# Performance work log

Measured on AMD Instinct MI355X. Metric: run time of the kernel, lower is better.

The kernel has to match this reference:

```python
import jax, jax.numpy as jnp
import numpy as np

B, N, C = 16, 577, 768
H = 12
HD = C // H            # 64 head dim
F = HD // 2            # 32 rotary frequency pairs
END = 24               # sqrt(N - 1): patch grid side
SCALE = HD ** -0.5


def setup_inputs() -> dict:
    key = jax.random.key(0)
    k0, k1, k2, k3 = jax.random.split(key, 4)
    x = jax.random.normal(k0, (B, N, C), jnp.float32)
    qkv_w = jax.random.normal(k1, (3 * C, C), jnp.float32) * 0.02
    proj_w = jax.random.normal(k2, (C, C), jnp.float32) * 0.02
    proj_b = jnp.zeros((C,), jnp.float32)
    # learnable mixed 2D RoPE frequencies, [2, H*F] as in init_2d_freqs().view(2,-1)
    freqs = jax.random.normal(k3, (2, H * F), jnp.float32) * 0.5
    return {"x": x, "qkv_w": qkv_w, "proj_w": proj_w, "proj_b": proj_b, "freqs": freqs}


def _rope_angles(freqs):
    # compute_mixed_cis: per-head angle = t_x*fx + t_y*fy over the 24x24 grid
    t = jnp.arange(END * END, dtype=jnp.float32)
    t_x = t % END
    t_y = jnp.floor(t / END)
    ang = t_x[:, None] * freqs[0][None, :] + t_y[:, None] * freqs[1][None, :]  # [Np, H*F]
    return ang.reshape(END * END, H, F).transpose(1, 0, 2)  # [H, Np, F]


def _apply_rope(q, cos, sin):
    # q: [B,H,Np,HD] viewed as complex pairs [B,H,Np,F,2]; rotate by e^{i*ang}
    qp = q.reshape(*q.shape[:-1], F, 2)
    re, im = qp[..., 0], qp[..., 1]
    out = jnp.stack([re * cos - im * sin, re * sin + im * cos], axis=-1)
    return out.reshape(q.shape)


def reference(x, qkv_w, proj_w, proj_b, freqs):
    qkv = (x @ qkv_w.T).reshape(B, N, 3, H, HD).transpose(2, 0, 3, 1, 4)
    q, k, v = qkv[0], qkv[1], qkv[2]              # each [B,H,N,HD]
    ang = _rope_angles(freqs)                      # [H, Np, F]
    cos = jnp.cos(ang)[None]                       # [1,H,Np,F]
    sin = jnp.sin(ang)[None]
    # CLS token (index 0) bypasses RoPE
    q = jnp.concatenate([q[:, :, :1], _apply_rope(q[:, :, 1:], cos, sin)], axis=2)
    k = jnp.concatenate([k[:, :, :1], _apply_rope(k[:, :, 1:], cos, sin)], axis=2)
    attn = jax.nn.softmax((q * SCALE) @ jnp.swapaxes(k, -2, -1), axis=-1)  # [B,H,N,N]
    out = (attn @ v).transpose(0, 2, 1, 3).reshape(B, N, C)
    return out @ proj_w.T + proj_b
```

## Files before the change

kernel.cpp:

```cpp
#include <hip/hip_runtime.h>


typedef __bf16 bf16;
typedef __bf16 bf16x4 __attribute__((ext_vector_type(4)));
typedef __bf16 bf16x8 __attribute__((ext_vector_type(8)));
typedef float f32x4 __attribute__((ext_vector_type(4)));

namespace {
constexpr int kC = 768;
constexpr int kNtok = 577;
constexpr int kM = 16 * kNtok;
constexpr int kMpad = 9472;
constexpr int kTok = 640;
constexpr int kBH = 192;
}

typedef __attribute__((address_space(3))) unsigned int as3_u32;
typedef __attribute__((address_space(1))) unsigned int as1_u32;
__device__ __forceinline__ void gl16(const bf16* g, bf16* l) {
  __builtin_amdgcn_global_load_lds((const as1_u32*)g, (as3_u32*)l, 16, 0, 0);
}

__device__ __forceinline__ int swz_lid(int hid, int nwg) {
  int q = nwg >> 3, r = nwg & 7;
  int x = hid & 7, y = hid >> 3;
  int base = (x < r) ? x * (q + 1) : r * (q + 1) + (x - r) * q;
  return base + y;
}

__global__ __launch_bounds__(256) void prep_kernel(
    const float* __restrict__ x, const float* __restrict__ qkv_w,
    const float* __restrict__ proj_w, const float* __restrict__ freqs,
    bf16* __restrict__ xb, bf16* __restrict__ wqb, bf16* __restrict__ pwb,
    float* __restrict__ cosT, float* __restrict__ sinT) {
  const int bidx = (int)blockIdx.x;
  const int tid = (int)threadIdx.x;
  if (bidx < 3552) {
    int idx = bidx * 256 + tid;
    int m = idx / 96, c8 = (idx % 96) * 8;
    bf16x8 o;
    if (m < kM) {
      const float* p = x + (size_t)m * kC + c8;
#pragma unroll
      for (int j = 0; j < 8; ++j) o[j] = (bf16)p[j];
    } else {
#pragma unroll
      for (int j = 0; j < 8; ++j) o[j] = (bf16)0.0f;
    }
    *(bf16x8*)(xb + (size_t)m * kC + c8) = o;
  } else if (bidx < 3552 + 864) {
    int off = ((bidx - 3552) * 256 + tid) * 8;
    bf16x8 o;
#pragma unroll
    for (int j = 0; j < 8; ++j) o[j] = (bf16)qkv_w[off + j];
    *(bf16x8*)(wqb + off) = o;
  } else if (bidx < 3552 + 864 + 288) {
    int off = ((bidx - 3552 - 864) * 256 + tid) * 8;
    bf16x8 o;
#pragma unroll
    for (int j = 0; j < 8; ++j) o[j] = (bf16)proj_w[off + j];
    *(bf16x8*)(pwb + off) = o;
  } else {
    int idx = (bidx - 3552 - 864 - 288) * 256 + tid;
    int f = idx & 31;
    int t = (idx >> 5) % 576;
    int h = idx / (576 * 32);
    float ang = (float)(t % 24) * freqs[h * 32 + f] + (float)(t / 24) * freqs[384 + h * 32 + f];
    float s, c;
    sincosf(ang, &s, &c);
    cosT[idx] = c;
    sinT[idx] = s;
  }
}

__global__ __launch_bounds__(512, 2) void qkv_gemm_kernel(
    const bf16* __restrict__ xb, const bf16* __restrict__ wb,
    const float* __restrict__ cosT, const float* __restrict__ sinT,
    bf16* __restrict__ qh, bf16* __restrict__ kbq, bf16* __restrict__ vb) {
  extern __shared__ __align__(16) char smem[];
  const int tid = (int)threadIdx.x;
  const int l = tid & 63, w = tid >> 6;
  const int lr = l & 15, lg = l >> 4;
  const int wm = w >> 2, wn = w & 3;
  const int w8 = w * 8;

  const int lid = swz_lid((int)blockIdx.x, 37 * 9);
  const int n0 = (lid % 9) * 256, m0 = (lid / 9) * 256;

  const int gch = (l & 7) ^ ((l >> 3) & 7);
  const bf16* aG = xb + (size_t)(m0 + w8 + (l >> 3)) * kC + gch * 8;
  const bf16* bG = wb + (size_t)(n0 + w8 + (l >> 3)) * kC + gch * 8;

  auto Abuf = [&](int b) { return (bf16*)(smem + b * 65536); };
  auto Bbuf = [&](int b) { return (bf16*)(smem + b * 65536 + 32768); };

  auto SA = [&](int b, int k0, int half) {
    bf16* A = Abuf(b);
    gl16(aG + (size_t)(half * 64) * kC + k0, A + (half * 64 + w8) * 64);
    gl16(aG + (size_t)(half * 64 + 128) * kC + k0, A + (half * 64 + 128 + w8) * 64);
  };
  auto SB = [&](int b, int k0, int bh) {
    bf16* B = Bbuf(b);
    const int base = w8 + (w8 & 32) + bh * 32;
    gl16(bG + (size_t)(base - w8) * kC + k0, B + base * 64);
    gl16(bG + (size_t)(base - w8 + 128) * kC + k0, B + (base + 128) * 64);
  };

  f32x4 acc[8][4];
  const f32x4 z = {0.f, 0.f, 0.f, 0.f};
#pragma unroll
  for (int mi = 0; mi < 8; ++mi)
#pragma unroll
    for (int ni = 0; ni < 4; ++ni) acc[mi][ni] = z;

  bf16x8 af[4][2], b0f[2][2], b1f[2][2];

  auto RDA = [&](int b, int H) {
    const bf16* A = Abuf(b);
#pragma unroll
    for (int mi = 0; mi < 4; ++mi) {
      const int row = wm * 128 + (H * 4 + mi) * 16 + lr;
#pragma unroll
      for (int kc = 0; kc < 2; ++kc)
        af[mi][kc] = *(const bf16x8*)&A[row * 64 + (((kc * 4 + lg) ^ (lr & 7)) << 3)];
    }
  };
  auto RDB = [&](int b, int Bs, bf16x8 (*dst)[2]) {
    const bf16* Bp = Bbuf(b);
#pragma unroll
    for (int nj = 0; nj < 2; ++nj) {
      const int row = wn * 64 + (Bs * 2 + nj) * 16 + lr;
#pragma unroll
      for (int kc = 0; kc < 2; ++kc)
        dst[nj][kc] = *(const bf16x8*)&Bp[row * 64 + (((kc * 4 + lg) ^ (lr & 7)) << 3)];
    }
  };
  auto MM = [&](int H, int Bs, bf16x8 (*bq)[2]) {
    __builtin_amdgcn_s_setprio(1);
#pragma unroll
    for (int kc = 0; kc < 2; ++kc)
#pragma unroll
      for (int mi = 0; mi < 4; ++mi)
#pragma unroll
        for (int nj = 0; nj < 2; ++nj)
          acc[H * 4 + mi][Bs * 2 + nj] = __builtin_amdgcn_mfma_f32_16x16x32_bf16(
              af[mi][kc], bq[nj][kc], acc[H * 4 + mi][Bs * 2 + nj], 0, 0, 0);
    __builtin_amdgcn_s_setprio(0);
  };
  auto BAR = [&](int n) {
    if (n == 0) asm volatile("s_waitcnt vmcnt(0)" ::: "memory");
    else if (n == 2) asm volatile("s_waitcnt vmcnt(2)" ::: "memory");
    else if (n == 4) asm volatile("s_waitcnt vmcnt(4)" ::: "memory");
    __builtin_amdgcn_sched_barrier(0);
    __builtin_amdgcn_s_barrier();
    __builtin_amdgcn_sched_barrier(0);
  };

  SA(0, 0, 0);
  SB(0, 0, 0);
  SB(0, 0, 1);
  SA(0, 0, 1);

#pragma unroll 1
  for (int t = 0; t < 11; ++t) {
    const int cb = t & 1, nb = cb ^ 1;
    const int k1 = (t + 1) * 64;
    BAR(4);  RDA(cb, 0); RDB(cb, 0, b0f); SA(nb, k1, 0); MM(0, 0, b0f);
    BAR(4);  RDB(cb, 1, b1f);             SB(nb, k1, 0); MM(0, 1, b1f);
    BAR(4);  RDA(cb, 1);                  SB(nb, k1, 1); MM(1, 1, b1f);
    BAR(-1); RDB(cb, 0, b0f);             SA(nb, k1, 1); MM(1, 0, b0f);
  }
  {
    const int cb = 1;
    BAR(4);  RDA(cb, 0); RDB(cb, 0, b0f); MM(0, 0, b0f);
    BAR(2);  RDB(cb, 1, b1f);             MM(0, 1, b1f);
    BAR(0);  RDA(cb, 1);                  MM(1, 1, b1f);
    BAR(-1); RDB(cb, 0, b0f);             MM(1, 0, b0f);
  }

  __builtin_amdgcn_sched_barrier(0);
  __syncthreads();
  float* tp = (float*)smem + w * 4096;
  const int nbase = n0 + wn * 64;
  const int which = nbase / kC;
  const int h = (nbase % kC) >> 6;
  bf16* dst = (which == 0) ? qh : (which == 1) ? kbq : vb;
  const float sc = (which == 0) ? 0.125f : 1.0f;
  const int c4 = lr * 4;
#pragma unroll
  for (int ch = 0; ch < 2; ++ch) {
#pragma unroll
    for (int mi = 0; mi < 4; ++mi)
#pragma unroll
      for (int ni = 0; ni < 4; ++ni)
#pragma unroll
        for (int r = 0; r < 4; ++r)
          tp[(mi * 16 + lg * 4 + r) * 64 + ni * 16 + lr] = acc[ch * 4 + mi][ni][r];
#pragma unroll
    for (int i = 0; i < 16; ++i) {
      const int row = i * 4 + lg;
      const int m = m0 + wm * 128 + ch * 64 + row;
      if (m >= kM) continue;
      float4 v4 = *(const float4*)&tp[row * 64 + c4];
      const int b = m / kNtok;
      const int tok = m - b * kNtok;
      float e0 = v4.x, o0 = v4.y, e1 = v4.z, o1 = v4.w;
      if (which < 2 && tok > 0) {
        const int tb = (h * 576 + tok - 1) * 32 + (c4 >> 1);
        float2 cc = *(const float2*)&cosT[tb];
        float2 ss = *(const float2*)&sinT[tb];
        float r0 = e0 * cc.x - o0 * ss.x, i0 = e0 * ss.x + o0 * cc.x;
        float r1 = e1 * cc.y - o1 * ss.y, i1 = e1 * ss.y + o1 * cc.y;
        e0 = r0; o0 = i0; e1 = r1; o1 = i1;
      }
      bf16x4 ov;
      ov[0] = (bf16)(e0 * sc); ov[1] = (bf16)(o0 * sc);
      ov[2] = (bf16)(e1 * sc); ov[3] = (bf16)(o1 * sc);
      *(bf16x4*)(dst + (((size_t)(b * 12 + h)) * kTok + tok) * 64 + c4) = ov;
    }
  }
}

__global__ __launch_bounds__(256) void vtrans_kernel(const bf16* __restrict__ vb,
                                                     bf16* __restrict__ vtb) {
  __shared__ __align__(16) bf16 T[64][72];
  const int bh = (int)blockIdx.x, s = (int)blockIdx.y;
  const int t = (int)threadIdx.x;
  const int row = t >> 2, qr = t & 3;
  const int tok = s * 64 + row;
  bf16x8 v0, v1;
  if (tok < kNtok) {
    const bf16* p = vb + ((size_t)bh * kTok + tok) * 64 + qr * 16;
    v0 = *(const bf16x8*)p;
    v1 = *(const bf16x8*)(p + 8);
  } else {
#pragma unroll
    for (int j = 0; j < 8; ++j) { v0[j] = (bf16)0.0f; v1[j] = (bf16)0.0f; }
  }
#pragma unroll
  for (int j = 0; j < 8; ++j) {
    T[qr * 16 + j][row] = v0[j];
    T[qr * 16 + 8 + j][row] = v1[j];
  }
  __syncthreads();
  const int d = row;
  bf16x8 o0 = *(const bf16x8*)&T[d][qr * 16];
  bf16x8 o1 = *(const bf16x8*)&T[d][qr * 16 + 8];
  bf16* dst = vtb + ((size_t)bh * 64 + d) * kTok + s * 64 + qr * 16;
  *(bf16x8*)dst = o0;
  *(bf16x8*)(dst + 8) = o1;
}

__global__ __launch_bounds__(512, 8) void attn_kernel(
    const bf16* __restrict__ qh, const bf16* __restrict__ kbq, const bf16* __restrict__ vtb,
    bf16* __restrict__ aoh) {
  __shared__ __align__(16) bf16 Ks[2][64 * 64];
  __shared__ __align__(16) bf16 Vs[2][64 * 64];
  __shared__ __align__(16) bf16 Ps[8][16 * 64];
  const int tid = (int)threadIdx.x;
  const int l = tid & 63, w = tid >> 6;
  const int lr = l & 15, lg = l >> 4;

  const int lid = swz_lid((int)blockIdx.x, 5 * kBH);
  const int bh = lid / 5, qt = lid - bh * 5;
  const int q0 = qt * 128;

  const int srow = w * 8 + (l >> 3);
  const int gch = (l & 7) ^ ((l >> 3) & 7);
  const bf16* kG = kbq + ((size_t)bh * kTok + srow) * 64 + gch * 8;
  const bf16* vG = vtb + ((size_t)bh * 64 + srow) * kTok + gch * 8;

  auto STAGE = [&](int buf, int j0) {
    gl16(kG + (size_t)j0 * 64, &Ks[buf][(w * 8) * 64]);
    gl16(vG + j0, &Vs[buf][(w * 8) * 64]);
  };

  bf16x8 qf[2];
  {
    const bf16* qp = qh + ((size_t)bh * kTok + (q0 + w * 16 + lr)) * 64 + lg * 8;
    qf[0] = *(const bf16x8*)qp;
    qf[1] = *(const bf16x8*)(qp + 32);
  }
  bf16x8 ones;
#pragma unroll
  for (int j = 0; j < 8; ++j) ones[j] = (bf16)1.0f;

  const f32x4 z = {0.f, 0.f, 0.f, 0.f};
  f32x4 o[4];
#pragma unroll
  for (int nf = 0; nf < 4; ++nf) o[nf] = z;
  f32x4 den = z;

  STAGE(0, 0);
#pragma unroll 1
  for (int jt = 0; jt < 9; ++jt) {
    const int cur = jt & 1;
    __syncthreads();
    if (jt < 8) STAGE(cur ^ 1, (jt + 1) * 64);

    f32x4 s[4];
#pragma unroll
    for (int ni = 0; ni < 4; ++ni) s[ni] = z;
    __builtin_amdgcn_s_setprio(1);
#pragma unroll
    for (int kc = 0; kc < 2; ++kc) {
#pragma unroll
      for (int ni = 0; ni < 4; ++ni) {
        int row = ni * 16 + lr;
        bf16x8 kf = *(const bf16x8*)&Ks[cur][row * 64 + (((kc * 4 + lg) ^ (row & 7)) << 3)];
        s[ni] = __builtin_amdgcn_mfma_f32_16x16x32_bf16(qf[kc], kf, s[ni], 0, 0, 0);
      }
    }
    __builtin_amdgcn_s_setprio(0);

#pragma unroll
    for (int ni = 0; ni < 4; ++ni)
#pragma unroll
      for (int r = 0; r < 4; ++r) {
        float p = __expf(s[ni][r]);
        int prow = lg * 4 + r;
        int pcol = ni * 16 + lr;
        Ps[w][prow * 64 + ((((pcol >> 3) ^ (prow & 7)) & 7) << 3) + (pcol & 7)] = (bf16)p;
      }

    __builtin_amdgcn_s_setprio(1);
#pragma unroll
    for (int kc = 0; kc < 2; ++kc) {
      bf16x8 pf = *(const bf16x8*)&Ps[w][lr * 64 + (((kc * 4 + lg) ^ (lr & 7)) << 3)];
      den = __builtin_amdgcn_mfma_f32_16x16x32_bf16(pf, ones, den, 0, 0, 0);
#pragma unroll
      for (int nf = 0; nf < 4; ++nf) {
        int row = nf * 16 + lr;
        bf16x8 vf = *(const bf16x8*)&Vs[cur][row * 64 + (((kc * 4 + lg) ^ (row & 7)) << 3)];
        o[nf] = __builtin_amdgcn_mfma_f32_16x16x32_bf16(pf, vf, o[nf], 0, 0, 0);
      }
    }
    __builtin_amdgcn_s_setprio(0);
  }

  {
    const bf16* k576 = kbq + ((size_t)bh * kTok + 576) * 64;
    bf16x8 ka = *(const bf16x8*)(k576 + lg * 8);
    bf16x8 kb2 = *(const bf16x8*)(k576 + 32 + lg * 8);
    float part = 0.f;
#pragma unroll
    for (int j = 0; j < 8; ++j)
      part += (float)qf[0][j] * (float)ka[j] + (float)qf[1][j] * (float)kb2[j];
    part += __shfl_xor(part, 16);
    part += __shfl_xor(part, 32);
    float v576[4];
#pragma unroll
    for (int nf = 0; nf < 4; ++nf)
      v576[nf] = (float)vtb[((size_t)bh * 64 + nf * 16 + lr) * kTok + 576];
#pragma unroll
    for (int r = 0; r < 4; ++r) {
      float p = __expf(__shfl(part, lg * 4 + r));
      den[r] += p;
#pragma unroll
      for (int nf = 0; nf < 4; ++nf) o[nf][r] += p * v576[nf];
    }
  }

  const int b = bh / 12, h = bh % 12;
#pragma unroll
  for (int r = 0; r < 4; ++r) {
    const int tok = q0 + w * 16 + lg * 4 + r;
    if (tok > 576) continue;
    const float inv = 1.0f / den[r];
    const size_t rowb = ((size_t)(b * kNtok + tok)) * kC + h * 64;
#pragma unroll
    for (int nf = 0; nf < 4; ++nf)
      aoh[rowb + nf * 16 + lr] = (bf16)(o[nf][r] * inv);
  }
}

__global__ __launch_bounds__(512, 4) void proj_gemm_kernel(
    const bf16* __restrict__ ah, const bf16* __restrict__ bw,
    const float* __restrict__ bias, float* __restrict__ out) {
  __shared__ __align__(16) char smem[65536];
  bf16* AsB = (bf16*)smem;
  bf16* BsB = (bf16*)(smem + 32768);
  const int tid = (int)threadIdx.x;
  const int l = tid & 63, w = tid >> 6;
  const int lr = l & 15, lg = l >> 4;
  const int wr = (w & 3) * 32, wc = (w >> 2) * 64;

  const int lid = swz_lid((int)blockIdx.x, 6 * 73);
  const int n0 = (lid % 6) * 128, m0 = (lid / 6) * 128;

  const int srow = w * 16 + (l >> 3);
  const int gch = (l & 7) ^ ((l >> 3) & 7);
  const bf16* aG = ah + (size_t)(m0 + srow) * kC + gch * 8;
  const bf16* bG = bw + (size_t)(n0 + srow) * kC + gch * 8;

  f32x4 acc[2][4];
  const f32x4 z = {0.f, 0.f, 0.f, 0.f};
#pragma unroll
  for (int mi = 0; mi < 2; ++mi)
#pragma unroll
    for (int ni = 0; ni < 4; ++ni) acc[mi][ni] = z;

  auto STAGE = [&](int buf, int k0) {
#pragma unroll
    for (int i = 0; i < 2; ++i) {
      gl16(aG + (size_t)i * 8 * kC + k0, &AsB[buf * 8192 + (w * 16 + i * 8) * 64]);
      gl16(bG + (size_t)i * 8 * kC + k0, &BsB[buf * 8192 + (w * 16 + i * 8) * 64]);
    }
  };
  auto COMPUTE = [&](int buf) {
    __builtin_amdgcn_s_setprio(1);
#pragma unroll
    for (int kc = 0; kc < 2; ++kc) {
      bf16x8 af[2], bfr[4];
#pragma unroll
      for (int ni = 0; ni < 4; ++ni) {
        int row = wc + ni * 16 + lr;
        bfr[ni] = *(const bf16x8*)&BsB[buf * 8192 + row * 64 + (((kc * 4 + lg) ^ (lr & 7)) << 3)];
      }
#pragma unroll
      for (int mi = 0; mi < 2; ++mi) {
        int row = wr + mi * 16 + lr;
        af[mi] = *(const bf16x8*)&AsB[buf * 8192 + row * 64 + (((kc * 4 + lg) ^ (lr & 7)) << 3)];
      }
#pragma unroll
      for (int mi = 0; mi < 2; ++mi)
#pragma unroll
        for (int ni = 0; ni < 4; ++ni)
          acc[mi][ni] = __builtin_amdgcn_mfma_f32_16x16x32_bf16(af[mi], bfr[ni], acc[mi][ni], 0, 0, 0);
    }
    __builtin_amdgcn_s_setprio(0);
  };

  STAGE(0, 0);
#pragma unroll 1
  for (int t = 0; t < 11; ++t) {
    const int buf = t & 1;
    STAGE(buf ^ 1, (t + 1) * 64);
    asm volatile("s_waitcnt vmcnt(4)" ::: "memory");
    __builtin_amdgcn_sched_barrier(0);
    __builtin_amdgcn_s_barrier();
    COMPUTE(buf);
    __builtin_amdgcn_s_barrier();
    __builtin_amdgcn_sched_barrier(0);
  }
  asm volatile("s_waitcnt vmcnt(0)" ::: "memory");
  __builtin_amdgcn_sched_barrier(0);
  __builtin_amdgcn_s_barrier();
  COMPUTE(1);

  __syncthreads();
  float* tp = (float*)smem + w * 2048;
#pragma unroll
  for (int mi = 0; mi < 2; ++mi)
#pragma unroll
    for (int ni = 0; ni < 4; ++ni)
#pragma unroll
      for (int r = 0; r < 4; ++r)
        tp[(mi * 16 + lg * 4 + r) * 64 + ni * 16 + lr] = acc[mi][ni][r];

  const int c4 = lr * 4;
  const int ncol = n0 + wc + c4;
  float4 bv = *(const float4*)&bias[ncol];
#pragma unroll
  for (int i = 0; i < 8; ++i) {
    const int row = i * 4 + lg;
    const int m = m0 + wr + row;
    if (m >= kM) continue;
    float4 v4 = *(const float4*)&tp[row * 64 + c4];
    v4.x += bv.x; v4.y += bv.y; v4.z += bv.z; v4.w += bv.w;
    *(float4*)(out + (size_t)m * kC + ncol) = v4;
  }
}

extern "C" void kernel_launch(void* const* d_in, const int* in_sizes, int n_in,
                              void* d_out, int out_size, void* d_ws, size_t ws_size,
                              hipStream_t stream) {
  const float* x = (const float*)d_in[0];
  const float* qkv_w = (const float*)d_in[1];
  const float* proj_w = (const float*)d_in[2];
  const float* proj_b = (const float*)d_in[3];
  const float* freqs = (const float*)d_in[4];
  float* out = (float*)d_out;

  static int qkv_smem_set = 0;
  if (!qkv_smem_set) {
    hipFuncSetAttribute((const void*)qkv_gemm_kernel,
                        hipFuncAttributeMaxDynamicSharedMemorySize, 131072);
    qkv_smem_set = 1;
  }

  char* p = (char*)d_ws;
  auto take = [&](size_t bytes) { char* r = p; p += (bytes + 255) & ~(size_t)255; return r; };
  float* cosT = (float*)take(221184 * 4);
  float* sinT = (float*)take(221184 * 4);
  bf16* xb   = (bf16*)take((size_t)kMpad * kC * 2);
  bf16* wqb  = (bf16*)take((size_t)2304 * kC * 2);
  bf16* pwb  = (bf16*)take((size_t)kC * kC * 2);
  bf16* qh   = (bf16*)take((size_t)kBH * kTok * 64 * 2);
  bf16* kbq  = (bf16*)take((size_t)kBH * kTok * 64 * 2);
  bf16* vb   = (bf16*)take((size_t)kBH * kTok * 64 * 2);
  bf16* vtb  = (bf16*)take((size_t)kBH * 64 * kTok * 2);
  bf16* aoh  = (bf16*)take((size_t)kMpad * kC * 2);

  prep_kernel<<<3552 + 864 + 288 + 864, 256, 0, stream>>>(
      x, qkv_w, proj_w, freqs, xb, wqb, pwb, cosT, sinT);
  qkv_gemm_kernel<<<dim3(37 * 9), 512, 131072, stream>>>(xb, wqb, cosT, sinT, qh, kbq, vb);
  vtrans_kernel<<<dim3(kBH, 10), 256, 0, stream>>>(vb, vtb);
  attn_kernel<<<dim3(5 * kBH), 512, 0, stream>>>(qh, kbq, vtb, aoh);
  proj_gemm_kernel<<<dim3(6 * 73), 512, 0, stream>>>(aoh, pwb, proj_b, out);
}
```

Measured before the change: 133.3 us.

## Retile QKV GEMM to 384x128 blocks with reworked load/barrier pipeline

Changes the QKV GEMM tile from 256x256 to 384x128, so the grid grows from 333 to 450 workgroups, and reassigns the 8 waves as 4x2 with 96x64 sub-tiles. The padded M dimension grows to 9600 so the new tile height divides it evenly. The main loop schedule is rewritten: LDS reads and global-to-LDS prefetches are issued before the barriers, and explicit lgkmcnt waits are placed before each MFMA group. The aim is better wave balance across the CUs and better overlap of loads with compute, at the cost of less B reuse per tile and more barriers per k-step.

```diff
diff --git a/kernel.cpp b/kernel.cpp
--- a/kernel.cpp
+++ b/kernel.cpp
@@ -10,7 +10,7 @@
 constexpr int kC = 768;
 constexpr int kNtok = 577;
 constexpr int kM = 16 * kNtok;
-constexpr int kMpad = 9472;
+constexpr int kMpadQ = 9600;
 constexpr int kTok = 640;
 constexpr int kBH = 192;
 }
@@ -35,7 +35,7 @@
     float* __restrict__ cosT, float* __restrict__ sinT) {
   const int bidx = (int)blockIdx.x;
   const int tid = (int)threadIdx.x;
-  if (bidx < 3552) {
+  if (bidx < 3600) {
     int idx = bidx * 256 + tid;
     int m = idx / 96, c8 = (idx % 96) * 8;
     bf16x8 o;
@@ -48,20 +48,20 @@
       for (int j = 0; j < 8; ++j) o[j] = (bf16)0.0f;
     }
     *(bf16x8*)(xb + (size_t)m * kC + c8) = o;
-  } else if (bidx < 3552 + 864) {
-    int off = ((bidx - 3552) * 256 + tid) * 8;
+  } else if (bidx < 3600 + 864) {
+    int off = ((bidx - 3600) * 256 + tid) * 8;
     bf16x8 o;
 #pragma unroll
     for (int j = 0; j < 8; ++j) o[j] = (bf16)qkv_w[off + j];
     *(bf16x8*)(wqb + off) = o;
-  } else if (bidx < 3552 + 864 + 288) {
-    int off = ((bidx - 3552 - 864) * 256 + tid) * 8;
+  } else if (bidx < 3600 + 864 + 288) {
+    int off = ((bidx - 3600 - 864) * 256 + tid) * 8;
     bf16x8 o;
 #pragma unroll
     for (int j = 0; j < 8; ++j) o[j] = (bf16)proj_w[off + j];
     *(bf16x8*)(pwb + off) = o;
   } else {
-    int idx = (bidx - 3552 - 864 - 288) * 256 + tid;
+    int idx = (bidx - 3600 - 864 - 288) * 256 + tid;
     int f = idx & 31;
     int t = (idx >> 5) % 576;
     int h = idx / (576 * 32);
@@ -81,73 +81,72 @@
   const int tid = (int)threadIdx.x;
   const int l = tid & 63, w = tid >> 6;
   const int lr = l & 15, lg = l >> 4;
-  const int wm = w >> 2, wn = w & 3;
+  const int wm = w >> 1, wn = w & 1;
   const int w8 = w * 8;
 
-  const int lid = swz_lid((int)blockIdx.x, 37 * 9);
-  const int n0 = (lid % 9) * 256, m0 = (lid / 9) * 256;
+  const int lid = swz_lid((int)blockIdx.x, 25 * 18);
+  const int n0 = (lid % 18) * 128, m0 = (lid / 18) * 384;
 
   const int gch = (l & 7) ^ ((l >> 3) & 7);
   const bf16* aG = xb + (size_t)(m0 + w8 + (l >> 3)) * kC + gch * 8;
   const bf16* bG = wb + (size_t)(n0 + w8 + (l >> 3)) * kC + gch * 8;
 
   auto Abuf = [&](int b) { return (bf16*)(smem + b * 65536); };
-  auto Bbuf = [&](int b) { return (bf16*)(smem + b * 65536 + 32768); };
-
-  auto SA = [&](int b, int k0, int half) {
-    bf16* A = Abuf(b);
-    gl16(aG + (size_t)(half * 64) * kC + k0, A + (half * 64 + w8) * 64);
-    gl16(aG + (size_t)(half * 64 + 128) * kC + k0, A + (half * 64 + 128 + w8) * 64);
-  };
-  auto SB = [&](int b, int k0, int bh) {
-    bf16* B = Bbuf(b);
-    const int base = w8 + (w8 & 32) + bh * 32;
-    gl16(bG + (size_t)(base - w8) * kC + k0, B + base * 64);
-    gl16(bG + (size_t)(base - w8 + 128) * kC + k0, B + (base + 128) * 64);
-  };
-
-  f32x4 acc[8][4];
+  auto Bbuf = [&](int b) { return (bf16*)(smem + b * 65536 + 49152); };
+
+  auto SA = [&](int b, int k0, int c) {
+    gl16(aG + (size_t)(c * 64) * kC + k0, Abuf(b) + (c * 64 + w8) * 64);
+  };
+  auto SB = [&](int b, int k0, int c) {
+    gl16(bG + (size_t)(c * 64) * kC + k0, Bbuf(b) + (c * 64 + w8) * 64);
+  };
+
+  f32x4 acc[6][4];
   const f32x4 z = {0.f, 0.f, 0.f, 0.f};
 #pragma unroll
-  for (int mi = 0; mi < 8; ++mi)
+  for (int mi = 0; mi < 6; ++mi)
 #pragma unroll
     for (int ni = 0; ni < 4; ++ni) acc[mi][ni] = z;
 
-  bf16x8 af[4][2], b0f[2][2], b1f[2][2];
-
-  auto RDA = [&](int b, int H) {
+  bf16x8 af[3][2], bf0[2][2], bf1[2][2];
+
+  auto RDA = [&](int b, int mih) {
     const bf16* A = Abuf(b);
 #pragma unroll
-    for (int mi = 0; mi < 4; ++mi) {
-      const int row = wm * 128 + (H * 4 + mi) * 16 + lr;
+    for (int mi = 0; mi < 3; ++mi) {
+      const int row = mih * 192 + wm * 48 + mi * 16 + lr;
 #pragma unroll
       for (int kc = 0; kc < 2; ++kc)
         af[mi][kc] = *(const bf16x8*)&A[row * 64 + (((kc * 4 + lg) ^ (lr & 7)) << 3)];
     }
   };
-  auto RDB = [&](int b, int Bs, bf16x8 (*dst)[2]) {
+  auto RDB = [&](int b, int nih, bf16x8 (&dst)[2][2]) {
     const bf16* Bp = Bbuf(b);
 #pragma unroll
-    for (int nj = 0; nj < 2; ++nj) {
-      const int row = wn * 64 + (Bs * 2 + nj) * 16 + lr;
+    for (int nl = 0; nl < 2; ++nl) {
+      const int row = wn * 64 + nih * 32 + nl * 16 + lr;
 #pragma unroll
       for (int kc = 0; kc < 2; ++kc)
-        dst[nj][kc] = *(const bf16x8*)&Bp[row * 64 + (((kc * 4 + lg) ^ (lr & 7)) << 3)];
-    }
-  };
-  auto MM = [&](int H, int Bs, bf16x8 (*bq)[2]) {
+        dst[nl][kc] = *(const bf16x8*)&Bp[row * 64 + (((kc * 4 + lg) ^ (lr & 7)) << 3)];
+    }
+  };
+  auto MM = [&](int mih, int nih, bf16x8 (&bq)[2][2]) {
     __builtin_amdgcn_s_setprio(1);
 #pragma unroll
     for (int kc = 0; kc < 2; ++kc)
 #pragma unroll
-      for (int mi = 0; mi < 4; ++mi)
-#pragma unroll
-        for (int nj = 0; nj < 2; ++nj)
-          acc[H * 4 + mi][Bs * 2 + nj] = __builtin_amdgcn_mfma_f32_16x16x32_bf16(
-              af[mi][kc], bq[nj][kc], acc[H * 4 + mi][Bs * 2 + nj], 0, 0, 0);
+      for (int mi = 0; mi < 3; ++mi)
+#pragma unroll
+        for (int nl = 0; nl < 2; ++nl)
+          acc[mih * 3 + mi][nih * 2 + nl] = __builtin_amdgcn_mfma_f32_16x16x32_bf16(
+              af[mi][kc], bq[nl][kc], acc[mih * 3 + mi][nih * 2 + nl], 0, 0, 0);
     __builtin_amdgcn_s_setprio(0);
   };
-  auto BAR = [&](int n) {
+  auto LGKM0 = [&]() {
+    asm volatile("s_waitcnt lgkmcnt(0)" ::: "memory");
+    __builtin_amdgcn_sched_barrier(0);
+  };
+  auto BARV = [&](int n) {
     if (n == 0) asm volatile("s_waitcnt vmcnt(0)" ::: "memory");
     else if (n == 2) asm volatile("s_waitcnt vmcnt(2)" ::: "memory");
     else if (n == 4) asm volatile("s_waitcnt vmcnt(4)" ::: "memory");
@@ -155,32 +154,45 @@
     __builtin_amdgcn_s_barrier();
     __builtin_amdgcn_sched_barrier(0);
   };
-
-  SA(0, 0, 0);
-  SB(0, 0, 0);
-  SB(0, 0, 1);
-  SA(0, 0, 1);
+  auto BAR = [&]() {
+    __builtin_amdgcn_sched_barrier(0);
+    __builtin_amdgcn_s_barrier();
+    __builtin_amdgcn_sched_barrier(0);
+  };
+
+  SA(0, 0, 0); SA(0, 0, 1);
+  SA(0, 0, 2); SB(0, 0, 0);
+  SA(0, 0, 3); SB(0, 0, 1);
+  SA(0, 0, 4); SA(0, 0, 5);
+  BARV(2);
 
 #pragma unroll 1
   for (int t = 0; t < 11; ++t) {
     const int cb = t & 1, nb = cb ^ 1;
     const int k1 = (t + 1) * 64;
-    BAR(4);  RDA(cb, 0); RDB(cb, 0, b0f); SA(nb, k1, 0); MM(0, 0, b0f);
-    BAR(4);  RDB(cb, 1, b1f);             SB(nb, k1, 0); MM(0, 1, b1f);
-    BAR(4);  RDA(cb, 1);                  SB(nb, k1, 1); MM(1, 1, b1f);
-    BAR(-1); RDB(cb, 0, b0f);             SA(nb, k1, 1); MM(1, 0, b0f);
+    RDA(cb, 0); RDB(cb, 0, bf0); SA(nb, k1, 0); SA(nb, k1, 1);
+    BAR(); LGKM0(); MM(0, 0, bf0); BAR();
+    RDB(cb, 1, bf1); SA(nb, k1, 2); SB(nb, k1, 0);
+    BARV(4); LGKM0(); MM(0, 1, bf1); BAR();
+    RDA(cb, 1); SA(nb, k1, 3); SB(nb, k1, 1);
+    BAR(); LGKM0(); MM(1, 1, bf1); BAR();
+    SA(nb, k1, 4); SA(nb, k1, 5);
+    BARV(2); LGKM0(); MM(1, 0, bf0); BAR();
   }
   {
     const int cb = 1;
-    BAR(4);  RDA(cb, 0); RDB(cb, 0, b0f); MM(0, 0, b0f);
-    BAR(2);  RDB(cb, 1, b1f);             MM(0, 1, b1f);
-    BAR(0);  RDA(cb, 1);                  MM(1, 1, b1f);
-    BAR(-1); RDB(cb, 0, b0f);             MM(1, 0, b0f);
+    RDA(cb, 0); RDB(cb, 0, bf0);
+    BAR(); LGKM0(); MM(0, 0, bf0); BAR();
+    RDB(cb, 1, bf1);
+    BARV(0); LGKM0(); MM(0, 1, bf1); BAR();
+    RDA(cb, 1);
+    BAR(); LGKM0(); MM(1, 1, bf1);
+    LGKM0(); MM(1, 0, bf0);
   }
 
   __builtin_amdgcn_sched_barrier(0);
   __syncthreads();
-  float* tp = (float*)smem + w * 4096;
+  float* tp = (float*)smem + w * 3072;
   const int nbase = n0 + wn * 64;
   const int which = nbase / kC;
   const int h = (nbase % kC) >> 6;
@@ -190,16 +202,16 @@
 #pragma unroll
   for (int ch = 0; ch < 2; ++ch) {
 #pragma unroll
-    for (int mi = 0; mi < 4; ++mi)
+    for (int mi = 0; mi < 3; ++mi)
 #pragma unroll
       for (int ni = 0; ni < 4; ++ni)
 #pragma unroll
         for (int r = 0; r < 4; ++r)
-          tp[(mi * 16 + lg * 4 + r) * 64 + ni * 16 + lr] = acc[ch * 4 + mi][ni][r];
-#pragma unroll
-    for (int i = 0; i < 16; ++i) {
+          tp[(mi * 16 + lg * 4 + r) * 64 + ni * 16 + lr] = acc[ch * 3 + mi][ni][r];
+#pragma unroll
+    for (int i = 0; i < 12; ++i) {
       const int row = i * 4 + lg;
-      const int m = m0 + wm * 128 + ch * 64 + row;
+      const int m = m0 + ch * 192 + wm * 48 + row;
       if (m >= kM) continue;
       float4 v4 = *(const float4*)&tp[row * 64 + c4];
       const int b = m / kNtok;
@@ -493,18 +505,18 @@
   auto take = [&](size_t bytes) { char* r = p; p += (bytes + 255) & ~(size_t)255; return r; };
   float* cosT = (float*)take(221184 * 4);
   float* sinT = (float*)take(221184 * 4);
-  bf16* xb   = (bf16*)take((size_t)kMpad * kC * 2);
+  bf16* xb   = (bf16*)take((size_t)kMpadQ * kC * 2);
   bf16* wqb  = (bf16*)take((size_t)2304 * kC * 2);
   bf16* pwb  = (bf16*)take((size_t)kC * kC * 2);
   bf16* qh   = (bf16*)take((size_t)kBH * kTok * 64 * 2);
   bf16* kbq  = (bf16*)take((size_t)kBH * kTok * 64 * 2);
   bf16* vb   = (bf16*)take((size_t)kBH * kTok * 64 * 2);
   bf16* vtb  = (bf16*)take((size_t)kBH * 64 * kTok * 2);
-  bf16* aoh  = (bf16*)take((size_t)kMpad * kC * 2);
-
-  prep_kernel<<<3552 + 864 + 288 + 864, 256, 0, stream>>>(
+  bf16* aoh  = (bf16*)take((size_t)9344 * kC * 2);
+
+  prep_kernel<<<3600 + 864 + 288 + 864, 256, 0, stream>>>(
       x, qkv_w, proj_w, freqs, xb, wqb, pwb, cosT, sinT);
-  qkv_gemm_kernel<<<dim3(37 * 9), 512, 131072, stream>>>(xb, wqb, cosT, sinT, qh, kbq, vb);
+  qkv_gemm_kernel<<<dim3(25 * 18), 512, 131072, stream>>>(xb, wqb, cosT, sinT, qh, kbq, vb);
   vtrans_kernel<<<dim3(kBH, 10), 256, 0, stream>>>(vb, vtb);
   attn_kernel<<<dim3(5 * kBH), 512, 0, stream>>>(qh, kbq, vtb, aoh);
   proj_gemm_kernel<<<dim3(6 * 73), 512, 0, stream>>>(aoh, pwb, proj_b, out);
```

After: 129.3 us. 1.03x faster.
